# Kernel optimization log

Hardware: AMD Instinct MI355X
Metric: run time of the kernel (lower is better)

The kernel has to match this reference:

```python
import jax, jax.numpy as jnp
import numpy as np

C_S = 384; C_Z = 256; HD = 16; NH = 12; NQ = 4; NV = 8; L = 512
WC = float(np.sqrt(2.0 / (9.0 * NQ)))
WL = float(np.sqrt(1.0 / 3.0))


def quat2rot(q):
    # q: [L,4] -> R: [L,3,3] (normalized quaternion to rotation matrix)
    q = q / jnp.linalg.norm(q, axis=-1, keepdims=True)
    w, x, y, z = q[..., 0], q[..., 1], q[..., 2], q[..., 3]
    R = jnp.stack([
        1 - 2 * (y * y + z * z), 2 * (x * y - w * z), 2 * (x * z + w * y),
        2 * (x * y + w * z), 1 - 2 * (x * x + z * z), 2 * (y * z - w * x),
        2 * (x * z - w * y), 2 * (y * z + w * x), 1 - 2 * (x * x + y * y)
    ], axis=-1)
    return R.reshape(q.shape[:-1] + (3, 3))


def _layer_norm(x, g, b, eps=1e-5):
    m = x.mean(-1, keepdims=True)
    v = x.var(-1, keepdims=True)
    return (x - m) / jnp.sqrt(v + eps) * g + b


def setup_inputs() -> dict:
    key = jax.random.key(0)
    ks = jax.random.split(key, 20)
    f32 = jnp.float32
    def w(k, shape, fan_in):
        return (jax.random.normal(k, shape) / np.sqrt(fan_in)).astype(f32)
    shid = NH * (C_Z + HD + NV * 3 + NV)  # 3648
    return {
        "s": jax.random.normal(ks[0], (1, L, C_S), f32),
        "z": jax.random.normal(ks[1], (1, L, L, C_Z), f32),
        "quat_tns": jax.random.normal(ks[2], (1, L, 4), f32),
        "trsl_tns": jax.random.normal(ks[3], (1, L, 3), f32),
        "Wq": w(ks[4], (C_S, NH * HD), C_S),
        "Wk": w(ks[5], (C_S, NH * HD), C_S),
        "Wv": w(ks[6], (C_S, NH * HD), C_S),
        "Wqp": w(ks[7], (C_S, NH * NQ * 3), C_S),
        "Wkp": w(ks[8], (C_S, NH * NQ * 3), C_S),
        "Wvp": w(ks[9], (C_S, NH * NV * 3), C_S),
        "Wb": w(ks[10], (C_Z, NH), C_Z),
        "Ws": w(ks[11], (shid, C_S), shid),
        "bs": jnp.zeros((C_S,), f32),
        "scale": jnp.full((NH,), np.log(np.e - 1.0), f32),
        "g1": jnp.ones((C_S,), f32), "b1": jnp.zeros((C_S,), f32),
        "Wm1": w(ks[12], (C_S, C_S), C_S), "bm1": jnp.zeros((C_S,), f32),
        "Wm2": w(ks[13], (C_S, C_S), C_S), "bm2": jnp.zeros((C_S,), f32),
        "Wm3": w(ks[14], (C_S, C_S), C_S), "bm3": jnp.zeros((C_S,), f32),
        "g2": jnp.ones((C_S,), f32), "b2": jnp.zeros((C_S,), f32),
    }


def reference(s, z, quat_tns, trsl_tns, Wq, Wk, Wv, Wqp, Wkp, Wvp, Wb, Ws, bs,
              scale, g1, b1, Wm1, bm1, Wm2, bm2, Wm3, bm3, g2, b2):
    N, Lr, _ = s.shape
    q = (s @ Wq).reshape(N, Lr, NH, HD)
    k = (s @ Wk).reshape(N, Lr, NH, HD)
    v = (s @ Wv).reshape(N, Lr, NH, HD)
    qp = (s @ Wqp).reshape(N, Lr, NH, NQ, 3)
    kp = (s @ Wkp).reshape(N, Lr, NH, NQ, 3)
    vp = (s @ Wvp).reshape(N, Lr, NH, NV, 3)
    b = z @ Wb                                   # [N,L,L,H]
    R = quat2rot(quat_tns[0])[None]              # [1,L,3,3]
    t = trsl_tns[:, :, None, None, :]            # [1,L,1,1,3]

    def fwd_trans(x):                            # global frame: R x + t
        return jnp.einsum('nlij,nlhpj->nlhpi', R, x) + t

    qpp = fwd_trans(qp)                          # [N,L,H,Q,3]
    kpp = fwd_trans(kp)
    vpp = fwd_trans(vp)                          # [N,L,H,V,3]

    # sum over points and coords of squared distances -> [N,L,L,H]
    d2 = jnp.sum((qpp[:, :, None] - kpp[:, None, :]) ** 2, axis=(-1, -2))
    qk = jnp.einsum('nihd,njhd->nijh', q, k) / np.sqrt(HD)
    qkp = 0.5 * WC * jax.nn.softplus(scale)[None, None, None, :] * d2
    a = jax.nn.softmax(WL * (qk + b - qkp), axis=2)  # softmax over keys j

    op = jnp.einsum('nijh,nijc->nihc', a, z)         # [N,L,H,C_Z]
    ov = jnp.einsum('nijh,njhd->nihd', a, v)         # [N,L,H,HD]
    ovp_g = jnp.einsum('nijh,njhp->nihp', a, vpp.reshape(N, Lr, NH, NV * 3))
    ovp_g = ovp_g.reshape(N, Lr, NH, NV, 3)
    # inverse transform: R^T (y - t)
    ovp = jnp.einsum('nlji,nlhvj->nlhvi', R, ovp_g - t)
    ovp_norm = jnp.linalg.norm(ovp, axis=-1)         # [N,L,H,V]

    shid = jnp.concatenate(
        [op, ov, ovp.reshape(N, Lr, NH, NV * 3), ovp_norm], axis=3
    ).reshape(N, Lr, -1)
    s1 = _layer_norm(s + shid @ Ws + bs, g1, b1)
    h = jax.nn.relu(s1 @ Wm1 + bm1)
    h = jax.nn.relu(h @ Wm2 + bm2)
    h = h @ Wm3 + bm3
    return _layer_norm(s1 + h, g2, b2)
```

## Files before the change

kernel.cpp:

```cpp
#include <hip/hip_runtime.h>
#include <math.h>

#define LSEQ 512
#define CS 384
#define CZ 256
#define HD 16
#define NH 12
#define NQ 4
#define NV 8
#define NALL 1152
#define SHID 3648
#define OFF_Q 0
#define OFF_K 192
#define OFF_V 384
#define OFF_QP 576
#define OFF_KP 720
#define OFF_VP 864

#define WC_CONST 0.2357022603955158f
#define WL_CONST 0.5773502691896258f

typedef __attribute__((ext_vector_type(8))) short bf16x8;
typedef __attribute__((ext_vector_type(4))) float f32x4;

__device__ __forceinline__ short f2bf(float f) {
  unsigned u = __builtin_bit_cast(unsigned, f);
  unsigned r = (u + 0x7FFF + ((u >> 16) & 1)) >> 16;
  return (short)r;
}

__global__ void k_prep(const float* quat, const float* trsl, const float* scale,
                       const float* Wb, float* R, float* T, float* CH,
                       unsigned short* WBP) {
  int t = threadIdx.x;
  if (t < LSEQ) {
    float w = quat[t*4+0], x = quat[t*4+1], y = quat[t*4+2], z = quat[t*4+3];
    float inv = 1.0f / sqrtf(w*w + x*x + y*y + z*z);
    w *= inv; x *= inv; y *= inv; z *= inv;
    float* r = R + t*9;
    r[0] = 1.f - 2.f*(y*y + z*z); r[1] = 2.f*(x*y - w*z);       r[2] = 2.f*(x*z + w*y);
    r[3] = 2.f*(x*y + w*z);       r[4] = 1.f - 2.f*(x*x + z*z); r[5] = 2.f*(y*z - w*x);
    r[6] = 2.f*(x*z - w*y);       r[7] = 2.f*(y*z + w*x);       r[8] = 1.f - 2.f*(x*x + y*y);
    T[t*3+0] = trsl[t*3+0]; T[t*3+1] = trsl[t*3+1]; T[t*3+2] = trsl[t*3+2];
  }
  if (t < NH) {
    float sc = scale[t];
    float sp = (sc > 20.f) ? sc : logf(1.f + expf(sc));
    CH[t] = 0.5f * WC_CONST * sp;
  }
  if (t < CZ) {
    #pragma unroll
    for (int h = 0; h < 16; h++)
      WBP[t*16 + h] = (h < NH) ? (unsigned short)f2bf(Wb[t*NH + h]) : (unsigned short)0;
  }
}

__global__ void k_concat(const float* Wq, const float* Wk, const float* Wv,
                         const float* Wqp, const float* Wkp, const float* Wvp,
                         float* Wcat) {
  int idx = blockIdx.x * 256 + threadIdx.x;
  if (idx >= CS * NALL) return;
  int r = idx / NALL, c = idx % NALL;
  float v;
  if (c < 192)       v = Wq [r*192 + c];
  else if (c < 384)  v = Wk [r*192 + (c-192)];
  else if (c < 576)  v = Wv [r*192 + (c-384)];
  else if (c < 720)  v = Wqp[r*144 + (c-576)];
  else if (c < 864)  v = Wkp[r*144 + (c-720)];
  else               v = Wvp[r*288 + (c-864)];
  Wcat[idx] = v;
}

__global__ __launch_bounds__(256) void k_gemm(
    const float* A, const float* B, float* C, const float* bias,
    int M, int N, int K, int lda, int ldb, int ldc,
    long strideA, long strideB, long strideC,
    int splitk, int relu, int reluA) {
  int zb = blockIdx.z;
  int batch = zb / splitk, ks = zb % splitk;
  A += (long)batch * strideA;
  B += (long)batch * strideB;
  C += (long)batch * strideC;
  int Ksub = K / splitk;
  int kbeg = ks * Ksub;

  __shared__ __align__(16) float As[16][68];
  __shared__ __align__(16) float Bs[16][68];
  int t = threadIdx.x;
  int m0 = blockIdx.y * 64, n0 = blockIdx.x * 64;
  int arow = t >> 2,  akq = (t & 3) * 4;
  int bkk  = t >> 4,  bnq = (t & 15) * 4;
  int ty = (t >> 4) * 4, tx = (t & 15) * 4;
  float acc[4][4];
  #pragma unroll
  for (int r = 0; r < 4; r++)
    #pragma unroll
    for (int c = 0; c < 4; c++) acc[r][c] = 0.f;

  for (int kb = kbeg; kb < kbeg + Ksub; kb += 16) {
    float4 av = *(const float4*)&A[(long)(m0 + arow) * lda + kb + akq];
    if (reluA) {
      av.x = fmaxf(av.x, 0.f); av.y = fmaxf(av.y, 0.f);
      av.z = fmaxf(av.z, 0.f); av.w = fmaxf(av.w, 0.f);
    }
    float4 bv;
    const float* brow = B + (long)(kb + bkk) * ldb;
    if (n0 + bnq + 3 < N) {
      bv = *(const float4*)&brow[n0 + bnq];
    } else {
      float tmp[4];
      #pragma unroll
      for (int u = 0; u < 4; u++) tmp[u] = (n0 + bnq + u < N) ? brow[n0 + bnq + u] : 0.f;
      bv = make_float4(tmp[0], tmp[1], tmp[2], tmp[3]);
    }
    __syncthreads();
    As[akq+0][arow] = av.x; As[akq+1][arow] = av.y;
    As[akq+2][arow] = av.z; As[akq+3][arow] = av.w;
    *(float4*)&Bs[bkk][bnq] = bv;
    __syncthreads();
    #pragma unroll
    for (int kk = 0; kk < 16; kk++) {
      float4 a4 = *(float4*)&As[kk][ty];
      float4 b4 = *(float4*)&Bs[kk][tx];
      acc[0][0] += a4.x*b4.x; acc[0][1] += a4.x*b4.y; acc[0][2] += a4.x*b4.z; acc[0][3] += a4.x*b4.w;
      acc[1][0] += a4.y*b4.x; acc[1][1] += a4.y*b4.y; acc[1][2] += a4.y*b4.z; acc[1][3] += a4.y*b4.w;
      acc[2][0] += a4.z*b4.x; acc[2][1] += a4.z*b4.y; acc[2][2] += a4.z*b4.z; acc[2][3] += a4.z*b4.w;
      acc[3][0] += a4.w*b4.x; acc[3][1] += a4.w*b4.y; acc[3][2] += a4.w*b4.z; acc[3][3] += a4.w*b4.w;
    }
  }

  if (splitk == 1) {
    #pragma unroll
    for (int r = 0; r < 4; r++) {
      int m = m0 + ty + r;
      #pragma unroll
      for (int c = 0; c < 4; c++) {
        int n = n0 + tx + c;
        if (n < N) {
          float v = acc[r][c] + (bias ? bias[n] : 0.f);
          if (relu) v = fmaxf(v, 0.f);
          C[(long)m * ldc + n] = v;
        }
      }
    }
  } else {
    #pragma unroll
    for (int r = 0; r < 4; r++) {
      int m = m0 + ty + r;
      #pragma unroll
      for (int c = 0; c < 4; c++) {
        int n = n0 + tx + c;
        if (n < N) {
          float v = acc[r][c] + ((ks == 0 && bias) ? bias[n] : 0.f);
          atomicAdd(&C[(long)m * ldc + n], v);
        }
      }
    }
  }
}

__global__ void k_trans(const float* P, const float* R, const float* T,
                        float* QPP, float* KT, float* KPT, float* VB) {
  int idx = blockIdx.x * 256 + threadIdx.x;
  if (idx >= LSEQ * NH) return;
  int h = idx / LSEQ, l = idx % LSEQ;
  const float* r = R + l*9;
  float t0 = T[l*3], t1 = T[l*3+1], t2 = T[l*3+2];
  const float* prow = P + (long)l * NALL;
  #pragma unroll
  for (int pq = 0; pq < NQ; pq++) {
    const float* x = prow + OFF_QP + h*12 + pq*3;
    float a = x[0], b = x[1], c = x[2];
    float* o = QPP + l*144 + h*12 + pq*3;
    o[0] = r[0]*a + r[1]*b + r[2]*c + t0;
    o[1] = r[3]*a + r[4]*b + r[5]*c + t1;
    o[2] = r[6]*a + r[7]*b + r[8]*c + t2;
  }
  #pragma unroll
  for (int d = 0; d < HD; d++)
    KT[(h*HD + d)*LSEQ + l] = prow[OFF_K + h*HD + d];
  #pragma unroll
  for (int pq = 0; pq < NQ; pq++) {
    const float* x = prow + OFF_KP + h*12 + pq*3;
    float a = x[0], b = x[1], c = x[2];
    KPT[(h*12 + pq*3 + 0)*LSEQ + l] = r[0]*a + r[1]*b + r[2]*c + t0;
    KPT[(h*12 + pq*3 + 1)*LSEQ + l] = r[3]*a + r[4]*b + r[5]*c + t1;
    KPT[(h*12 + pq*3 + 2)*LSEQ + l] = r[6]*a + r[7]*b + r[8]*c + t2;
  }
  float* vb = VB + ((long)(h * LSEQ + l)) * 40;
  #pragma unroll
  for (int d = 0; d < 16; d++) vb[d] = prow[OFF_V + h*16 + d];
  #pragma unroll
  for (int pv = 0; pv < NV; pv++) {
    const float* x = prow + OFF_VP + h*24 + pv*3;
    float a = x[0], b = x[1], c = x[2];
    vb[16 + 3*pv + 0] = r[0]*a + r[1]*b + r[2]*c + t0;
    vb[16 + 3*pv + 1] = r[3]*a + r[4]*b + r[5]*c + t1;
    vb[16 + 3*pv + 2] = r[6]*a + r[7]*b + r[8]*c + t2;
  }
}

__global__ __launch_bounds__(256) void k_bias_mfma(const float* zin,
    const unsigned short* WBP, float* Bb) {
  int i = blockIdx.x;
  int part = blockIdx.y;
  int t = threadIdx.x;
  int w = t >> 6, l = t & 63;
  int r = l & 15, kg = l >> 4;

  bf16x8 bfrag[8];
  #pragma unroll
  for (int kt = 0; kt < 8; kt++) {
    #pragma unroll
    for (int jj = 0; jj < 8; jj++) {
      int c = kt*32 + kg*8 + jj;
      bfrag[kt][jj] = (short)WBP[c*16 + r];
    }
  }

  #pragma unroll
  for (int tt = 0; tt < 2; tt++) {
    int j0 = part*128 + (w*2 + tt)*16;
    const float* zrow = zin + ((long)i*LSEQ + j0 + r) * CZ + kg*8;
    f32x4 acc = {0.f, 0.f, 0.f, 0.f};
    #pragma unroll
    for (int kt = 0; kt < 8; kt++) {
      float4 z0 = *(const float4*)(zrow + kt*32);
      float4 z1 = *(const float4*)(zrow + kt*32 + 4);
      bf16x8 af;
      af[0] = f2bf(z0.x); af[1] = f2bf(z0.y); af[2] = f2bf(z0.z); af[3] = f2bf(z0.w);
      af[4] = f2bf(z1.x); af[5] = f2bf(z1.y); af[6] = f2bf(z1.z); af[7] = f2bf(z1.w);
      acc = __builtin_amdgcn_mfma_f32_16x16x32_bf16(af, bfrag[kt], acc, 0, 0, 0);
    }
    if (r < NH) {
      int jbase = j0 + kg*4;
      float4 o = make_float4(acc[0], acc[1], acc[2], acc[3]);
      *(float4*)&Bb[((long)i*NH + r)*LSEQ + jbase] = o;
    }
  }
}

#define AI 2
__global__ __launch_bounds__(512) void k_attn3(const float* P, const float* QPP,
    const float* KT, const float* KPT, const float* Bb, const float* CH, float* Aa) {
  int i0 = blockIdx.x * AI;
  int t = threadIdx.x, w = t >> 6, j = t;
  __shared__ float reds[2][8][AI];
  __shared__ float bcs[2][AI];
  float lg[AI];
  for (int h = 0; h < NH; h++) {
    int pb = h & 1;
    float kreg[16];
    #pragma unroll
    for (int d = 0; d < 16; d++) kreg[d] = KT[(h*16 + d)*LSEQ + j];
    float kp[12];
    #pragma unroll
    for (int p = 0; p < 12; p++) kp[p] = KPT[(h*12 + p)*LSEQ + j];
    float ch = CH[h];
    #pragma unroll
    for (int ii = 0; ii < AI; ii++) {
      const float* q  = P + (long)(i0+ii)*NALL + OFF_Q + h*HD;
      const float* qp = QPP + (i0+ii)*144 + h*12;
      float dot = 0.f;
      #pragma unroll
      for (int d = 0; d < 16; d++) dot += q[d] * kreg[d];
      float d2 = 0.f;
      #pragma unroll
      for (int p = 0; p < 12; p++) { float dd = qp[p] - kp[p]; d2 += dd*dd; }
      float bb = Bb[((long)(i0+ii)*NH + h)*LSEQ + j];
      lg[ii] = __expf(WL_CONST * (0.25f*dot + bb - ch*d2));
    }
    #pragma unroll
    for (int ii = 0; ii < AI; ii++) {
      float sv = lg[ii];
      #pragma unroll
      for (int off = 32; off >= 1; off >>= 1) sv += __shfl_xor(sv, off);
      if ((t & 63) == 0) reds[pb][w][ii] = sv;
    }
    __syncthreads();
    if (t < AI) {
      float sv = 0.f;
      #pragma unroll
      for (int u = 0; u < 8; u++) sv += reds[pb][u][t];
      bcs[pb][t] = 1.0f / sv;
    }
    __syncthreads();
    #pragma unroll
    for (int ii = 0; ii < AI; ii++)
      Aa[((long)(i0+ii)*NH + h)*LSEQ + j] = lg[ii] * bcs[pb][ii];
  }
}

__global__ __launch_bounds__(256) void k_op2(const float* zin, const float* Aa, float* SH) {
  int i = blockIdx.x, t = threadIdx.x;
  const float* ab = Aa + (long)i * NH * LSEQ;
  const float* zrow = zin + (long)i * LSEQ * CZ + t;
  float acc[NH];
  #pragma unroll
  for (int h = 0; h < NH; h++) acc[h] = 0.f;
  for (int j = 0; j < LSEQ; j += 4) {
    float z0 = zrow[(long)(j+0) * CZ];
    float z1 = zrow[(long)(j+1) * CZ];
    float z2 = zrow[(long)(j+2) * CZ];
    float z3 = zrow[(long)(j+3) * CZ];
    #pragma unroll
    for (int h = 0; h < NH; h++) {
      float4 a4 = *(const float4*)&ab[h * LSEQ + j];
      acc[h] += a4.x*z0 + a4.y*z1 + a4.z*z2 + a4.w*z3;
    }
  }
  float* sh = SH + (long)i * SHID + t;
  #pragma unroll
  for (int h = 0; h < NH; h++) sh[h * 304] = acc[h];
}

__global__ void k_ovp(const float* OVT, const float* R, const float* T, float* SH) {
  int idx = blockIdx.x * 256 + threadIdx.x;
  if (idx >= LSEQ * NH) return;
  int l = idx / NH, h = idx % NH;
  const float* o = OVT + ((long)(h * LSEQ + l)) * 40;
  float* sh = SH + (long)l * SHID + h * 304;
  #pragma unroll
  for (int d = 0; d < 16; d++) sh[256 + d] = o[d];
  const float* r = R + l*9;
  float t0 = T[l*3], t1 = T[l*3+1], t2 = T[l*3+2];
  #pragma unroll
  for (int v = 0; v < NV; v++) {
    float a = o[16+3*v+0] - t0, b = o[16+3*v+1] - t1, c = o[16+3*v+2] - t2;
    float x = r[0]*a + r[3]*b + r[6]*c;
    float y = r[1]*a + r[4]*b + r[7]*c;
    float zz= r[2]*a + r[5]*b + r[8]*c;
    sh[272 + 3*v + 0] = x;
    sh[272 + 3*v + 1] = y;
    sh[272 + 3*v + 2] = zz;
    sh[296 + v] = sqrtf(x*x + y*y + zz*zz);
  }
}

__global__ __launch_bounds__(384) void k_ln(const float* res, const float* y,
                                            const float* g, const float* b, float* out) {
  int l = blockIdx.x, t = threadIdx.x;
  __shared__ float red1[6], red2[6];
  __shared__ float mv[2];
  float x = res[(long)l * CS + t] + y[(long)l * CS + t];
  float s = x, s2 = x * x;
  #pragma unroll
  for (int off = 32; off >= 1; off >>= 1) { s += __shfl_xor(s, off); s2 += __shfl_xor(s2, off); }
  if ((t & 63) == 0) { red1[t >> 6] = s; red2[t >> 6] = s2; }
  __syncthreads();
  if (t == 0) {
    float ss = 0.f, ss2 = 0.f;
    #pragma unroll
    for (int u = 0; u < 6; u++) { ss += red1[u]; ss2 += red2[u]; }
    float m = ss / CS;
    float var = ss2 / CS - m * m;
    mv[0] = m; mv[1] = 1.0f / sqrtf(var + 1e-5f);
  }
  __syncthreads();
  out[(long)l * CS + t] = (x - mv[0]) * mv[1] * g[t] + b[t];
}

extern "C" void kernel_launch(void* const* d_in, const int* in_sizes, int n_in,
                              void* d_out, int out_size, void* d_ws, size_t ws_size,
                              hipStream_t stream) {
  const float* s    = (const float*)d_in[0];
  const float* z    = (const float*)d_in[1];
  const float* quat = (const float*)d_in[2];
  const float* trsl = (const float*)d_in[3];
  const float* Wq   = (const float*)d_in[4];
  const float* Wk   = (const float*)d_in[5];
  const float* Wv   = (const float*)d_in[6];
  const float* Wqp  = (const float*)d_in[7];
  const float* Wkp  = (const float*)d_in[8];
  const float* Wvp  = (const float*)d_in[9];
  const float* Wb   = (const float*)d_in[10];
  const float* Ws   = (const float*)d_in[11];
  const float* bs   = (const float*)d_in[12];
  const float* scale= (const float*)d_in[13];
  const float* g1   = (const float*)d_in[14];
  const float* b1   = (const float*)d_in[15];
  const float* Wm1  = (const float*)d_in[16];
  const float* bm1  = (const float*)d_in[17];
  const float* Wm2  = (const float*)d_in[18];
  const float* bm2  = (const float*)d_in[19];
  const float* Wm3  = (const float*)d_in[20];
  const float* bm3  = (const float*)d_in[21];
  const float* g2   = (const float*)d_in[22];
  const float* b2   = (const float*)d_in[23];
  float* out = (float*)d_out;

  float* p = (float*)d_ws;
  float* R    = p; p += 512*9;
  float* T    = p; p += 512*3;
  float* CH   = p; p += 16;
  unsigned short* WBP = (unsigned short*)p; p += (CZ*16)/2;
  float* Wcat = p; p += (long)CS*NALL;
  float* P    = p; p += (long)LSEQ*NALL;
  float* QPP  = p; p += LSEQ*144;
  float* KT   = p; p += NH*HD*LSEQ;
  float* KPT  = p; p += NH*12*LSEQ;
  float* VB   = p; p += (long)NH*LSEQ*40;
  float* Bb   = p; p += (long)LSEQ*NH*LSEQ;
  float* OVT  = p; p += (long)NH*LSEQ*40;
  float* SH   = p; p += (long)LSEQ*SHID;
  float* T1   = p; p += LSEQ*CS;
  float* S1   = p; p += LSEQ*CS;
  float* H1   = p; p += LSEQ*CS;
  float* H2   = p; p += LSEQ*CS;
  float* H3   = p; p += LSEQ*CS;
  float* Aa   = Bb;

  k_prep<<<1, 512, 0, stream>>>(quat, trsl, scale, Wb, R, T, CH, WBP);
  k_concat<<<(CS*NALL + 255)/256, 256, 0, stream>>>(Wq, Wk, Wv, Wqp, Wkp, Wvp, Wcat);
  k_gemm<<<dim3(NALL/64, LSEQ/64, 1), 256, 0, stream>>>(
      s, Wcat, P, nullptr, LSEQ, NALL, CS, CS, NALL, NALL, 0, 0, 0, 1, 0, 0);
  k_trans<<<(LSEQ*NH + 255)/256, 256, 0, stream>>>(P, R, T, QPP, KT, KPT, VB);
  k_bias_mfma<<<dim3(LSEQ, 4), 256, 0, stream>>>(z, WBP, Bb);
  k_attn3<<<LSEQ/AI, 512, 0, stream>>>(P, QPP, KT, KPT, Bb, CH, Aa);
  k_op2<<<LSEQ, 256, 0, stream>>>(z, Aa, SH);
  k_gemm<<<dim3(1, LSEQ/64, NH), 256, 0, stream>>>(
      Aa, VB, OVT, nullptr, LSEQ, 40, LSEQ,
      NH*LSEQ, 40, 40, 512, (long)LSEQ*40, (long)LSEQ*40, 1, 0, 0);
  k_ovp<<<(LSEQ*NH + 255)/256, 256, 0, stream>>>(OVT, R, T, SH);
  hipMemsetAsync(T1, 0, (size_t)LSEQ*CS*sizeof(float), stream);
  hipMemsetAsync(H1, 0, (size_t)LSEQ*CS*sizeof(float), stream);
  hipMemsetAsync(H2, 0, (size_t)LSEQ*CS*sizeof(float), stream);
  hipMemsetAsync(H3, 0, (size_t)LSEQ*CS*sizeof(float), stream);
  k_gemm<<<dim3(CS/64, LSEQ/64, 6), 256, 0, stream>>>(
      SH, Ws, T1, bs, LSEQ, CS, SHID, SHID, CS, CS, 0, 0, 0, 6, 0, 0);
  k_ln<<<LSEQ, CS, 0, stream>>>(s, T1, g1, b1, S1);
  k_gemm<<<dim3(CS/64, LSEQ/64, 4), 256, 0, stream>>>(
      S1, Wm1, H1, bm1, LSEQ, CS, CS, CS, CS, CS, 0, 0, 0, 4, 0, 0);
  k_gemm<<<dim3(CS/64, LSEQ/64, 4), 256, 0, stream>>>(
      H1, Wm2, H2, bm2, LSEQ, CS, CS, CS, CS, CS, 0, 0, 0, 4, 0, 1);
  k_gemm<<<dim3(CS/64, LSEQ/64, 4), 256, 0, stream>>>(
      H2, Wm3, H3, bm3, LSEQ, CS, CS, CS, CS, CS, 0, 0, 0, 4, 0, 1);
  k_ln<<<LSEQ, CS, 0, stream>>>(S1, H3, g2, b2, out);
}
```

Baseline: 789.3 us.

## Fuse pair-bias MFMA, softmax and z/value aggregation; prefetch GEMM tiles and raise split-K

The pair-bias MFMA, exponentiation, softmax normalisation and the z-weighted and value-weighted aggregations now run in one per-query kernel. Each z row is streamed only for the bias and the aggregation, and the bias and attention matrices are no longer written to or read from memory. Logits without the bias are computed separately. Softmax drops the max subtraction and relies on unnormalised exp sums, which risks overflow. The GEMM gains register prefetching of the next K tile, loses its N-bounds checks and batching, and uses higher split-K factors, with a single memset covering all atomically accumulated buffers.

```diff
diff --git a/kernel.cpp b/kernel.cpp
--- a/kernel.cpp
+++ b/kernel.cpp
@@ -73,16 +73,10 @@
 
 __global__ __launch_bounds__(256) void k_gemm(
     const float* A, const float* B, float* C, const float* bias,
-    int M, int N, int K, int lda, int ldb, int ldc,
-    long strideA, long strideB, long strideC,
-    int splitk, int relu, int reluA) {
-  int zb = blockIdx.z;
-  int batch = zb / splitk, ks = zb % splitk;
-  A += (long)batch * strideA;
-  B += (long)batch * strideB;
-  C += (long)batch * strideC;
+    int K, int lda, int ldb, int ldc, int splitk, int relu, int reluA) {
+  int ks = blockIdx.z;
   int Ksub = K / splitk;
-  int kbeg = ks * Ksub;
+  int kbeg = ks * Ksub, kend = kbeg + Ksub;
 
   __shared__ __align__(16) float As[16][68];
   __shared__ __align__(16) float Bs[16][68];
@@ -97,27 +91,26 @@
     #pragma unroll
     for (int c = 0; c < 4; c++) acc[r][c] = 0.f;
 
-  for (int kb = kbeg; kb < kbeg + Ksub; kb += 16) {
-    float4 av = *(const float4*)&A[(long)(m0 + arow) * lda + kb + akq];
+  const float* aptr  = A + (long)(m0 + arow) * lda + akq;
+  const float* bbase = B + n0 + bnq;
+  float4 av = *(const float4*)&aptr[kbeg];
+  float4 bv = *(const float4*)&bbase[(long)(kbeg + bkk) * ldb];
+
+  for (int kb = kbeg; kb < kend; kb += 16) {
+    float4 a_cur = av, b_cur = bv;
     if (reluA) {
-      av.x = fmaxf(av.x, 0.f); av.y = fmaxf(av.y, 0.f);
-      av.z = fmaxf(av.z, 0.f); av.w = fmaxf(av.w, 0.f);
-    }
-    float4 bv;
-    const float* brow = B + (long)(kb + bkk) * ldb;
-    if (n0 + bnq + 3 < N) {
-      bv = *(const float4*)&brow[n0 + bnq];
-    } else {
-      float tmp[4];
-      #pragma unroll
-      for (int u = 0; u < 4; u++) tmp[u] = (n0 + bnq + u < N) ? brow[n0 + bnq + u] : 0.f;
-      bv = make_float4(tmp[0], tmp[1], tmp[2], tmp[3]);
+      a_cur.x = fmaxf(a_cur.x, 0.f); a_cur.y = fmaxf(a_cur.y, 0.f);
+      a_cur.z = fmaxf(a_cur.z, 0.f); a_cur.w = fmaxf(a_cur.w, 0.f);
     }
     __syncthreads();
-    As[akq+0][arow] = av.x; As[akq+1][arow] = av.y;
-    As[akq+2][arow] = av.z; As[akq+3][arow] = av.w;
-    *(float4*)&Bs[bkk][bnq] = bv;
+    As[akq+0][arow] = a_cur.x; As[akq+1][arow] = a_cur.y;
+    As[akq+2][arow] = a_cur.z; As[akq+3][arow] = a_cur.w;
+    *(float4*)&Bs[bkk][bnq] = b_cur;
     __syncthreads();
+    if (kb + 16 < kend) {
+      av = *(const float4*)&aptr[kb + 16];
+      bv = *(const float4*)&bbase[(long)(kb + 16 + bkk) * ldb];
+    }
     #pragma unroll
     for (int kk = 0; kk < 16; kk++) {
       float4 a4 = *(float4*)&As[kk][ty];
@@ -136,11 +129,9 @@
       #pragma unroll
       for (int c = 0; c < 4; c++) {
         int n = n0 + tx + c;
-        if (n < N) {
-          float v = acc[r][c] + (bias ? bias[n] : 0.f);
-          if (relu) v = fmaxf(v, 0.f);
-          C[(long)m * ldc + n] = v;
-        }
+        float v = acc[r][c] + (bias ? bias[n] : 0.f);
+        if (relu) v = fmaxf(v, 0.f);
+        C[(long)m * ldc + n] = v;
       }
     }
   } else {
@@ -150,78 +141,128 @@
       #pragma unroll
       for (int c = 0; c < 4; c++) {
         int n = n0 + tx + c;
-        if (n < N) {
-          float v = acc[r][c] + ((ks == 0 && bias) ? bias[n] : 0.f);
-          atomicAdd(&C[(long)m * ldc + n], v);
-        }
+        float v = acc[r][c] + ((ks == 0 && bias) ? bias[n] : 0.f);
+        atomicAdd(&C[(long)m * ldc + n], v);
       }
     }
   }
 }
 
 __global__ void k_trans(const float* P, const float* R, const float* T,
-                        float* QPP, float* KT, float* KPT, float* VB) {
+                        float* QPP, float* KT, float* KPT, float* VBT) {
+  int task = blockIdx.y;
   int idx = blockIdx.x * 256 + threadIdx.x;
   if (idx >= LSEQ * NH) return;
   int h = idx / LSEQ, l = idx % LSEQ;
   const float* r = R + l*9;
   float t0 = T[l*3], t1 = T[l*3+1], t2 = T[l*3+2];
   const float* prow = P + (long)l * NALL;
-  #pragma unroll
-  for (int pq = 0; pq < NQ; pq++) {
-    const float* x = prow + OFF_QP + h*12 + pq*3;
-    float a = x[0], b = x[1], c = x[2];
-    float* o = QPP + l*144 + h*12 + pq*3;
-    o[0] = r[0]*a + r[1]*b + r[2]*c + t0;
-    o[1] = r[3]*a + r[4]*b + r[5]*c + t1;
-    o[2] = r[6]*a + r[7]*b + r[8]*c + t2;
-  }
-  #pragma unroll
-  for (int d = 0; d < HD; d++)
-    KT[(h*HD + d)*LSEQ + l] = prow[OFF_K + h*HD + d];
-  #pragma unroll
-  for (int pq = 0; pq < NQ; pq++) {
-    const float* x = prow + OFF_KP + h*12 + pq*3;
-    float a = x[0], b = x[1], c = x[2];
-    KPT[(h*12 + pq*3 + 0)*LSEQ + l] = r[0]*a + r[1]*b + r[2]*c + t0;
-    KPT[(h*12 + pq*3 + 1)*LSEQ + l] = r[3]*a + r[4]*b + r[5]*c + t1;
-    KPT[(h*12 + pq*3 + 2)*LSEQ + l] = r[6]*a + r[7]*b + r[8]*c + t2;
-  }
-  float* vb = VB + ((long)(h * LSEQ + l)) * 40;
-  #pragma unroll
-  for (int d = 0; d < 16; d++) vb[d] = prow[OFF_V + h*16 + d];
-  #pragma unroll
-  for (int pv = 0; pv < NV; pv++) {
-    const float* x = prow + OFF_VP + h*24 + pv*3;
-    float a = x[0], b = x[1], c = x[2];
-    vb[16 + 3*pv + 0] = r[0]*a + r[1]*b + r[2]*c + t0;
-    vb[16 + 3*pv + 1] = r[3]*a + r[4]*b + r[5]*c + t1;
-    vb[16 + 3*pv + 2] = r[6]*a + r[7]*b + r[8]*c + t2;
-  }
-}
-
-__global__ __launch_bounds__(256) void k_bias_mfma(const float* zin,
-    const unsigned short* WBP, float* Bb) {
-  int i = blockIdx.x;
-  int part = blockIdx.y;
-  int t = threadIdx.x;
+  if (task == 0) {
+    #pragma unroll
+    for (int pq = 0; pq < NQ; pq++) {
+      const float* x = prow + OFF_QP + h*12 + pq*3;
+      float a = x[0], b = x[1], c = x[2];
+      float* o = QPP + l*144 + h*12 + pq*3;
+      o[0] = r[0]*a + r[1]*b + r[2]*c + t0;
+      o[1] = r[3]*a + r[4]*b + r[5]*c + t1;
+      o[2] = r[6]*a + r[7]*b + r[8]*c + t2;
+    }
+    #pragma unroll
+    for (int d = 0; d < HD; d++)
+      KT[(h*HD + d)*LSEQ + l] = prow[OFF_K + h*HD + d];
+  } else if (task == 1) {
+    #pragma unroll
+    for (int pq = 0; pq < NQ; pq++) {
+      const float* x = prow + OFF_KP + h*12 + pq*3;
+      float a = x[0], b = x[1], c = x[2];
+      KPT[(h*12 + pq*3 + 0)*LSEQ + l] = r[0]*a + r[1]*b + r[2]*c + t0;
+      KPT[(h*12 + pq*3 + 1)*LSEQ + l] = r[3]*a + r[4]*b + r[5]*c + t1;
+      KPT[(h*12 + pq*3 + 2)*LSEQ + l] = r[6]*a + r[7]*b + r[8]*c + t2;
+    }
+  } else {
+    #pragma unroll
+    for (int d = 0; d < 16; d++)
+      VBT[((long)(h*40 + d))*LSEQ + l] = prow[OFF_V + h*16 + d];
+    #pragma unroll
+    for (int pv = 0; pv < NV; pv++) {
+      const float* x = prow + OFF_VP + h*24 + pv*3;
+      float a = x[0], b = x[1], c = x[2];
+      VBT[((long)(h*40 + 16 + 3*pv + 0))*LSEQ + l] = r[0]*a + r[1]*b + r[2]*c + t0;
+      VBT[((long)(h*40 + 16 + 3*pv + 1))*LSEQ + l] = r[3]*a + r[4]*b + r[5]*c + t1;
+      VBT[((long)(h*40 + 16 + 3*pv + 2))*LSEQ + l] = r[6]*a + r[7]*b + r[8]*c + t2;
+    }
+  }
+}
+
+#define AI 2
+__global__ __launch_bounds__(512) void k_logit(const float* P, const float* QPP,
+    const float* KT, const float* KPT, const float* CH, float* LG) {
+  int i0 = blockIdx.x * AI;
+  int t = threadIdx.x, j = t;
+  #pragma unroll
+  for (int h = 0; h < NH; h++) {
+    float kreg[16];
+    #pragma unroll
+    for (int d = 0; d < 16; d++) kreg[d] = KT[(h*16 + d)*LSEQ + j];
+    float kp[12];
+    #pragma unroll
+    for (int p = 0; p < 12; p++) kp[p] = KPT[(h*12 + p)*LSEQ + j];
+    float ch = CH[h];
+    #pragma unroll
+    for (int ii = 0; ii < AI; ii++) {
+      const float* q  = P + (long)(i0+ii)*NALL + OFF_Q + h*HD;
+      const float* qp = QPP + (i0+ii)*144 + h*12;
+      float dot = 0.f;
+      #pragma unroll
+      for (int d = 0; d < 16; d++) dot += q[d] * kreg[d];
+      float d2 = 0.f;
+      #pragma unroll
+      for (int p = 0; p < 12; p++) { float dd = qp[p] - kp[p]; d2 += dd*dd; }
+      LG[((long)(i0+ii)*NH + h)*LSEQ + j] = WL_CONST * (0.25f*dot - ch*d2);
+    }
+  }
+}
+
+__global__ __launch_bounds__(256) void k_fused(const float* zin,
+    const unsigned short* WBP, const float* LG, const float* VBT,
+    float* SH, float* OVT) {
+  __shared__ __align__(16) float lgs[NH][520];
+  __shared__ __align__(16) float es[NH][68];
+  __shared__ float sred[4][NH];
+  __shared__ float ssum[NH];
+  int i = blockIdx.x, t = threadIdx.x;
   int w = t >> 6, l = t & 63;
   int r = l & 15, kg = l >> 4;
 
+  const float* lgsrc = LG + (long)i * NH * LSEQ;
+  #pragma unroll
+  for (int idx = t; idx < NH*LSEQ/4; idx += 256) {
+    int h = idx >> 7, q4 = idx & 127;
+    *(float4*)&lgs[h][q4*4] = *(const float4*)&lgsrc[h*LSEQ + q4*4];
+  }
+
   bf16x8 bfrag[8];
   #pragma unroll
-  for (int kt = 0; kt < 8; kt++) {
-    #pragma unroll
-    for (int jj = 0; jj < 8; jj++) {
-      int c = kt*32 + kg*8 + jj;
-      bfrag[kt][jj] = (short)WBP[c*16 + r];
-    }
-  }
-
-  #pragma unroll
-  for (int tt = 0; tt < 2; tt++) {
-    int j0 = part*128 + (w*2 + tt)*16;
-    const float* zrow = zin + ((long)i*LSEQ + j0 + r) * CZ + kg*8;
+  for (int kt = 0; kt < 8; kt++)
+    #pragma unroll
+    for (int jj = 0; jj < 8; jj++)
+      bfrag[kt][jj] = (short)WBP[(kt*32 + kg*8 + jj)*16 + r];
+
+  float accop[NH];
+  #pragma unroll
+  for (int h = 0; h < NH; h++) accop[h] = 0.f;
+  int pair0 = t, pair1 = t + 256;
+  int h0 = pair0 / 40, p0 = pair0 % 40;
+  int h1 = pair1 / 40, p1 = pair1 % 40;
+  float accv0 = 0.f, accv1 = 0.f;
+  float sparts = 0.f;
+  int hh = (r < NH) ? r : 0;
+
+  __syncthreads();
+
+  for (int jt = 0; jt < LSEQ; jt += 64) {
+    int j0 = jt + w*16;
+    const float* zrow = zin + ((long)i*LSEQ + j0 + r)*CZ + kg*8;
     f32x4 acc = {0.f, 0.f, 0.f, 0.f};
     #pragma unroll
     for (int kt = 0; kt < 8; kt++) {
@@ -232,93 +273,70 @@
       af[4] = f2bf(z1.x); af[5] = f2bf(z1.y); af[6] = f2bf(z1.z); af[7] = f2bf(z1.w);
       acc = __builtin_amdgcn_mfma_f32_16x16x32_bf16(af, bfrag[kt], acc, 0, 0, 0);
     }
+    float4 lgv = *(float4*)&lgs[hh][j0 + kg*4];
+    float e0 = __expf(lgv.x + WL_CONST*acc[0]);
+    float e1 = __expf(lgv.y + WL_CONST*acc[1]);
+    float e2 = __expf(lgv.z + WL_CONST*acc[2]);
+    float e3 = __expf(lgv.w + WL_CONST*acc[3]);
     if (r < NH) {
-      int jbase = j0 + kg*4;
-      float4 o = make_float4(acc[0], acc[1], acc[2], acc[3]);
-      *(float4*)&Bb[((long)i*NH + r)*LSEQ + jbase] = o;
-    }
-  }
-}
-
-#define AI 2
-__global__ __launch_bounds__(512) void k_attn3(const float* P, const float* QPP,
-    const float* KT, const float* KPT, const float* Bb, const float* CH, float* Aa) {
-  int i0 = blockIdx.x * AI;
-  int t = threadIdx.x, w = t >> 6, j = t;
-  __shared__ float reds[2][8][AI];
-  __shared__ float bcs[2][AI];
-  float lg[AI];
-  for (int h = 0; h < NH; h++) {
-    int pb = h & 1;
-    float kreg[16];
-    #pragma unroll
-    for (int d = 0; d < 16; d++) kreg[d] = KT[(h*16 + d)*LSEQ + j];
-    float kp[12];
-    #pragma unroll
-    for (int p = 0; p < 12; p++) kp[p] = KPT[(h*12 + p)*LSEQ + j];
-    float ch = CH[h];
-    #pragma unroll
-    for (int ii = 0; ii < AI; ii++) {
-      const float* q  = P + (long)(i0+ii)*NALL + OFF_Q + h*HD;
-      const float* qp = QPP + (i0+ii)*144 + h*12;
-      float dot = 0.f;
-      #pragma unroll
-      for (int d = 0; d < 16; d++) dot += q[d] * kreg[d];
-      float d2 = 0.f;
-      #pragma unroll
-      for (int p = 0; p < 12; p++) { float dd = qp[p] - kp[p]; d2 += dd*dd; }
-      float bb = Bb[((long)(i0+ii)*NH + h)*LSEQ + j];
-      lg[ii] = __expf(WL_CONST * (0.25f*dot + bb - ch*d2));
-    }
-    #pragma unroll
-    for (int ii = 0; ii < AI; ii++) {
-      float sv = lg[ii];
-      #pragma unroll
-      for (int off = 32; off >= 1; off >>= 1) sv += __shfl_xor(sv, off);
-      if ((t & 63) == 0) reds[pb][w][ii] = sv;
+      sparts += e0 + e1 + e2 + e3;
+      *(float4*)&es[r][w*16 + kg*4] = make_float4(e0, e1, e2, e3);
     }
     __syncthreads();
-    if (t < AI) {
-      float sv = 0.f;
-      #pragma unroll
-      for (int u = 0; u < 8; u++) sv += reds[pb][u][t];
-      bcs[pb][t] = 1.0f / sv;
+    const float* zc = zin + ((long)i*LSEQ + jt)*CZ + t;
+    #pragma unroll 4
+    for (int jj = 0; jj < 64; jj += 4) {
+      float z0 = zc[(jj+0)*CZ], z1 = zc[(jj+1)*CZ];
+      float z2 = zc[(jj+2)*CZ], z3 = zc[(jj+3)*CZ];
+      #pragma unroll
+      for (int h = 0; h < NH; h++) {
+        float4 ev = *(float4*)&es[h][jj];
+        accop[h] += ev.x*z0 + ev.y*z1 + ev.z*z2 + ev.w*z3;
+      }
+    }
+    {
+      const float* vb0 = VBT + ((long)pair0)*LSEQ + jt;
+      #pragma unroll
+      for (int jj = 0; jj < 64; jj += 4) {
+        float4 vv = *(const float4*)&vb0[jj];
+        float4 ev = *(float4*)&es[h0][jj];
+        accv0 += vv.x*ev.x + vv.y*ev.y + vv.z*ev.z + vv.w*ev.w;
+      }
+      if (pair1 < 480) {
+        const float* vb1 = VBT + ((long)pair1)*LSEQ + jt;
+        #pragma unroll
+        for (int jj = 0; jj < 64; jj += 4) {
+          float4 vv = *(const float4*)&vb1[jj];
+          float4 ev = *(float4*)&es[h1][jj];
+          accv1 += vv.x*ev.x + vv.y*ev.y + vv.z*ev.z + vv.w*ev.w;
+        }
+      }
     }
     __syncthreads();
-    #pragma unroll
-    for (int ii = 0; ii < AI; ii++)
-      Aa[((long)(i0+ii)*NH + h)*LSEQ + j] = lg[ii] * bcs[pb][ii];
-  }
-}
-
-__global__ __launch_bounds__(256) void k_op2(const float* zin, const float* Aa, float* SH) {
-  int i = blockIdx.x, t = threadIdx.x;
-  const float* ab = Aa + (long)i * NH * LSEQ;
-  const float* zrow = zin + (long)i * LSEQ * CZ + t;
-  float acc[NH];
-  #pragma unroll
-  for (int h = 0; h < NH; h++) acc[h] = 0.f;
-  for (int j = 0; j < LSEQ; j += 4) {
-    float z0 = zrow[(long)(j+0) * CZ];
-    float z1 = zrow[(long)(j+1) * CZ];
-    float z2 = zrow[(long)(j+2) * CZ];
-    float z3 = zrow[(long)(j+3) * CZ];
-    #pragma unroll
-    for (int h = 0; h < NH; h++) {
-      float4 a4 = *(const float4*)&ab[h * LSEQ + j];
-      acc[h] += a4.x*z0 + a4.y*z1 + a4.z*z2 + a4.w*z3;
-    }
-  }
+  }
+
+  sparts += __shfl_xor(sparts, 16);
+  sparts += __shfl_xor(sparts, 32);
+  if (l < NH) sred[w][l] = sparts;
+  __syncthreads();
+  if (t < NH) {
+    float sv = sred[0][t] + sred[1][t] + sred[2][t] + sred[3][t];
+    ssum[t] = 1.0f / sv;
+  }
+  __syncthreads();
+
   float* sh = SH + (long)i * SHID + t;
   #pragma unroll
-  for (int h = 0; h < NH; h++) sh[h * 304] = acc[h];
+  for (int h = 0; h < NH; h++) sh[h * 304] = accop[h] * ssum[h];
+  OVT[(long)i*480 + pair0] = accv0 * ssum[h0];
+  if (pair1 < 480) OVT[(long)i*480 + pair1] = accv1 * ssum[h1];
 }
 
 __global__ void k_ovp(const float* OVT, const float* R, const float* T, float* SH) {
   int idx = blockIdx.x * 256 + threadIdx.x;
   if (idx >= LSEQ * NH) return;
   int l = idx / NH, h = idx % NH;
-  const float* o = OVT + ((long)(h * LSEQ + l)) * 40;
+  const float* o = OVT + (long)l*480 + h*40;
   float* sh = SH + (long)l * SHID + h * 304;
   #pragma unroll
   for (int d = 0; d < 16; d++) sh[256 + d] = o[d];
@@ -395,45 +413,39 @@
   float* CH   = p; p += 16;
   unsigned short* WBP = (unsigned short*)p; p += (CZ*16)/2;
   float* Wcat = p; p += (long)CS*NALL;
-  float* P    = p; p += (long)LSEQ*NALL;
   float* QPP  = p; p += LSEQ*144;
   float* KT   = p; p += NH*HD*LSEQ;
   float* KPT  = p; p += NH*12*LSEQ;
-  float* VB   = p; p += (long)NH*LSEQ*40;
-  float* Bb   = p; p += (long)LSEQ*NH*LSEQ;
-  float* OVT  = p; p += (long)NH*LSEQ*40;
+  float* VBT  = p; p += (long)NH*40*LSEQ;
+  float* LG   = p; p += (long)LSEQ*NH*LSEQ;
+  float* OVT  = p; p += (long)LSEQ*480;
   float* SH   = p; p += (long)LSEQ*SHID;
+  float* S1   = p; p += LSEQ*CS;
+  float* ZB   = p;
+  float* P    = p; p += (long)LSEQ*NALL;
   float* T1   = p; p += LSEQ*CS;
-  float* S1   = p; p += LSEQ*CS;
   float* H1   = p; p += LSEQ*CS;
   float* H2   = p; p += LSEQ*CS;
   float* H3   = p; p += LSEQ*CS;
-  float* Aa   = Bb;
-
+  size_t zbytes = ((size_t)LSEQ*NALL + 4*LSEQ*CS) * sizeof(float);
+
+  hipMemsetAsync(ZB, 0, zbytes, stream);
   k_prep<<<1, 512, 0, stream>>>(quat, trsl, scale, Wb, R, T, CH, WBP);
   k_concat<<<(CS*NALL + 255)/256, 256, 0, stream>>>(Wq, Wk, Wv, Wqp, Wkp, Wvp, Wcat);
-  k_gemm<<<dim3(NALL/64, LSEQ/64, 1), 256, 0, stream>>>(
-      s, Wcat, P, nullptr, LSEQ, NALL, CS, CS, NALL, NALL, 0, 0, 0, 1, 0, 0);
-  k_trans<<<(LSEQ*NH + 255)/256, 256, 0, stream>>>(P, R, T, QPP, KT, KPT, VB);
-  k_bias_mfma<<<dim3(LSEQ, 4), 256, 0, stream>>>(z, WBP, Bb);
-  k_attn3<<<LSEQ/AI, 512, 0, stream>>>(P, QPP, KT, KPT, Bb, CH, Aa);
-  k_op2<<<LSEQ, 256, 0, stream>>>(z, Aa, SH);
-  k_gemm<<<dim3(1, LSEQ/64, NH), 256, 0, stream>>>(
-      Aa, VB, OVT, nullptr, LSEQ, 40, LSEQ,
-      NH*LSEQ, 40, 40, 512, (long)LSEQ*40, (long)LSEQ*40, 1, 0, 0);
+  k_gemm<<<dim3(NALL/64, LSEQ/64, 2), 256, 0, stream>>>(
+      s, Wcat, P, nullptr, CS, CS, NALL, NALL, 2, 0, 0);
+  k_trans<<<dim3(24, 3), 256, 0, stream>>>(P, R, T, QPP, KT, KPT, VBT);
+  k_logit<<<LSEQ/AI, 512, 0, stream>>>(P, QPP, KT, KPT, CH, LG);
+  k_fused<<<LSEQ, 256, 0, stream>>>(z, WBP, LG, VBT, SH, OVT);
   k_ovp<<<(LSEQ*NH + 255)/256, 256, 0, stream>>>(OVT, R, T, SH);
-  hipMemsetAsync(T1, 0, (size_t)LSEQ*CS*sizeof(float), stream);
-  hipMemsetAsync(H1, 0, (size_t)LSEQ*CS*sizeof(float), stream);
-  hipMemsetAsync(H2, 0, (size_t)LSEQ*CS*sizeof(float), stream);
-  hipMemsetAsync(H3, 0, (size_t)LSEQ*CS*sizeof(float), stream);
-  k_gemm<<<dim3(CS/64, LSEQ/64, 6), 256, 0, stream>>>(
-      SH, Ws, T1, bs, LSEQ, CS, SHID, SHID, CS, CS, 0, 0, 0, 6, 0, 0);
+  k_gemm<<<dim3(CS/64, LSEQ/64, 12), 256, 0, stream>>>(
+      SH, Ws, T1, bs, SHID, SHID, CS, CS, 12, 0, 0);
   k_ln<<<LSEQ, CS, 0, stream>>>(s, T1, g1, b1, S1);
-  k_gemm<<<dim3(CS/64, LSEQ/64, 4), 256, 0, stream>>>(
-      S1, Wm1, H1, bm1, LSEQ, CS, CS, CS, CS, CS, 0, 0, 0, 4, 0, 0);
-  k_gemm<<<dim3(CS/64, LSEQ/64, 4), 256, 0, stream>>>(
-      H1, Wm2, H2, bm2, LSEQ, CS, CS, CS, CS, CS, 0, 0, 0, 4, 0, 1);
-  k_gemm<<<dim3(CS/64, LSEQ/64, 4), 256, 0, stream>>>(
-      H2, Wm3, H3, bm3, LSEQ, CS, CS, CS, CS, CS, 0, 0, 0, 4, 0, 1);
+  k_gemm<<<dim3(CS/64, LSEQ/64, 8), 256, 0, stream>>>(
+      S1, Wm1, H1, bm1, CS, CS, CS, CS, 8, 0, 0);
+  k_gemm<<<dim3(CS/64, LSEQ/64, 8), 256, 0, stream>>>(
+      H1, Wm2, H2, bm2, CS, CS, CS, CS, 8, 0, 1);
+  k_gemm<<<dim3(CS/64, LSEQ/64, 8), 256, 0, stream>>>(
+      H2, Wm3, H3, bm3, CS, CS, CS, CS, 8, 0, 1);
   k_ln<<<LSEQ, CS, 0, stream>>>(S1, H3, g2, b2, out);
 }
```

Result: faster. 689.2 us (-12.7%).
